# Optimization experiments

Measured on AMD Instinct MI355X. Metric: run time of the kernel, lower is better.

The kernel has to match this reference:

```python
import jax, jax.numpy as jnp
import numpy as np

MARKER = 50251
BETA_FLOOR = 0.1
LOCAL_SCALE = 0.3
EPS = 1e-6
WINDOW = 256

B, T, D, H, K, V = 4, 1024, 1024, 16, 64, 64
HD = D // H  # SWA head dim


def setup_inputs() -> dict:
    key = jax.random.key(0)
    ks = jax.random.split(key, 16)
    p = lambda i, shape: jax.random.normal(ks[i], shape, jnp.float32) * 0.02
    return dict(
        x=jax.random.normal(ks[0], (B, T, D), jnp.float32),
        initial_state=jnp.zeros((B, H, K, V), jnp.float32),
        W_k=p(1, (D, H * K)),
        W_v=p(2, (D, H * V)),
        W_gdn_o=p(3, (H * V, D)),
        W_beta=p(4, (D, H)), b_beta=jnp.full((H,), -2.0, jnp.float32),
        W_g=p(5, (D, H)), b_g=jnp.full((H,), 2.0, jnp.float32),
        W_lq=p(6, (D, D)), W_lk=p(7, (D, D)), W_lv=p(8, (D, D)),
        W_swa_o=p(9, (D, D)),
        W_ret_o=p(10, (H * V, D)),
        W_gate=p(11, (D, H)), b_gate=jnp.ones((H,), jnp.float32),
        norm_w=jnp.ones((D,), jnp.float32),
        input_ids=jax.random.randint(ks[12], (B, T), 0, 50257, jnp.int32),
    )


def _delta_scan(k, v, beta, g, S0):
    # gated delta rule:  Sd = g_t * S_{t-1};  S_t = Sd + beta_t * k_t (v_t - k_t Sd);  o_t = k_t S_t
    # k:[B,Tm,H,K]  v:[B,Tm,H,V]  beta,g:[B,Tm,H]  S0:[B,H,K,V]
    def step(S, inp):
        kt, vt, bt, gt = inp  # [B,H,K],[B,H,V],[B,H],[B,H]
        Sd = gt[..., None, None] * S
        err = vt - jnp.einsum('bhk,bhkv->bhv', kt, Sd)
        Sn = Sd + bt[..., None, None] * (kt[..., None] * err[:, :, None, :])
        ot = jnp.einsum('bhk,bhkv->bhv', kt, Sn)
        return Sn, ot
    Sf, o = jax.lax.scan(step, S0, (k.transpose(1, 0, 2, 3), v.transpose(1, 0, 2, 3),
                                    beta.transpose(1, 0, 2), g.transpose(1, 0, 2)))
    return o.transpose(1, 0, 2, 3), Sf  # [B,Tm,H,V], [B,H,K,V]


def _forward(x, initial_state, W_k, W_v, W_gdn_o, W_beta, b_beta, W_g, b_g,
             W_lq, W_lk, W_lv, W_swa_o, W_ret_o, W_gate, b_gate, norm_w, input_ids):
    # RMSNorm
    rms = jnp.sqrt(jnp.mean(x * x, axis=-1, keepdims=True) + EPS)
    xn = x / rms * norm_w

    # shared L2-normalized keys and values
    k_shared = (xn @ W_k).reshape(B, T, H, K)
    k_shared = k_shared / jnp.maximum(jnp.linalg.norm(k_shared, axis=-1, keepdims=True), 1e-12)
    v_full = (xn @ W_v).reshape(B, T, H, V)

    # shifted-value GDN inputs (predict next token's value)
    k = k_shared[:, :-1]
    v = v_full[:, 1:]
    beta = jax.nn.sigmoid(xn[:, :-1] @ W_beta + b_beta)  # [B,T-1,H]
    g = jax.nn.sigmoid(xn[:, :-1] @ W_g + b_g)
    marker = (input_ids[:, :-1] == MARKER)[..., None]
    beta = beta * (BETA_FLOOR + (1.0 - BETA_FLOOR) * marker.astype(beta.dtype))

    o, Sf = _delta_scan(k, v, beta, g, initial_state)
    gdn_out = jnp.concatenate([jnp.zeros((B, 1, H, V), o.dtype), o], axis=1)
    gdn_out = gdn_out.reshape(B, T, H * V) @ W_gdn_o  # [B,T,D]

    # sliding-window attention (fallback masked-softmax path)
    q = (xn @ W_lq).reshape(B, T, H, HD).transpose(0, 2, 1, 3)
    kl = (xn @ W_lk).reshape(B, T, H, HD).transpose(0, 2, 1, 3)
    vl = (xn @ W_lv).reshape(B, T, H, HD).transpose(0, 2, 1, 3)
    scale = K ** (-0.5)
    i = jnp.arange(T)[:, None]
    j = jnp.arange(T)[None, :]
    allowed = (j <= i) & (j >= i - WINDOW)  # causal within window
    attn = jnp.einsum('bhqd,bhkd->bhqk', q, kl) * scale
    attn = jnp.where(allowed, attn, -jnp.inf)
    probs = jax.nn.softmax(attn, axis=-1)
    local = jnp.einsum('bhqk,bhkd->bhqd', probs, vl).transpose(0, 2, 1, 3).reshape(B, T, D)
    local_out = LOCAL_SCALE * (local @ W_swa_o)  # eval mode

    # retrieval from final state with shared keys as queries
    retrieved = jnp.einsum('bhkv,bthk->bthv', Sf, k_shared).reshape(B, T, H * V)
    retrieval_out = retrieved @ W_ret_o
    gate = jax.nn.sigmoid(xn @ W_gate + b_gate)  # [B,T,H]
    retrieval_out = jnp.mean(gate, axis=-1, keepdims=True) * retrieval_out

    return x + gdn_out + local_out + retrieval_out


def reference(x, initial_state, W_k, W_v, W_gdn_o, W_beta, b_beta, W_g, b_g,
              W_lq, W_lk, W_lv, W_swa_o, W_ret_o, W_gate, b_gate, norm_w, input_ids):
    return _forward(x, initial_state, W_k, W_v, W_gdn_o, W_beta, b_beta, W_g, b_g,
                    W_lq, W_lk, W_lv, W_swa_o, W_ret_o, W_gate, b_gate, norm_w, input_ids)
```

## Files before the change

kernel.cpp:

```cpp
#include <hip/hip_runtime.h>
#include <hip/hip_bf16.h>

#define BB 4
#define TT 1024
#define DD 1024
#define HH 16
#define KK 64
#define VV 64
#define WIN 256
#define MARKER_ID 50251
#define PSA 5120
#define PSB 3072
#define NPROJ 5248

typedef short bfrag8 __attribute__((ext_vector_type(8)));
typedef float f32x4 __attribute__((ext_vector_type(4)));

static __device__ __forceinline__ unsigned short f2bf(float f) {
  __hip_bfloat16 h = __float2bfloat16(f);
  union { __hip_bfloat16 h; unsigned short u; } cv;
  cv.h = h;
  return cv.u;
}
static __device__ __forceinline__ float bf2f(unsigned short u) {
  union { unsigned int i; float f; } c;
  c.i = ((unsigned int)u) << 16;
  return c.f;
}
static __device__ __forceinline__ void gld_lds16(const unsigned short* g,
                                                 unsigned short* l) {
  __builtin_amdgcn_global_load_lds(
      (const __attribute__((address_space(1))) void*)g,
      (__attribute__((address_space(3))) void*)l, 16, 0, 0);
}

__global__ __launch_bounds__(256) void rmsnorm_kernel(
    const float* __restrict__ x, const float* __restrict__ nw,
    unsigned short* __restrict__ xnb) {
  int row = blockIdx.x;
  int tid = threadIdx.x;
  const float4* xr = (const float4*)(x + (size_t)row * DD);
  float4 v = xr[tid];
  float ss = v.x * v.x + v.y * v.y + v.z * v.z + v.w * v.w;
#pragma unroll
  for (int off = 32; off; off >>= 1) ss += __shfl_xor(ss, off);
  __shared__ float red[4];
  int wid = tid >> 6;
  if ((tid & 63) == 0) red[wid] = ss;
  __syncthreads();
  float tot = red[0] + red[1] + red[2] + red[3];
  float inv = 1.0f / sqrtf(tot * (1.0f / DD) + 1e-6f);
  const float4* wr = (const float4*)nw;
  float4 wv = wr[tid];
  ushort4 o;
  o.x = f2bf(v.x * inv * wv.x);
  o.y = f2bf(v.y * inv * wv.y);
  o.z = f2bf(v.z * inv * wv.z);
  o.w = f2bf(v.w * inv * wv.w);
  *(ushort4*)&xnb[(size_t)row * DD + tid * 4] = o;
}

__global__ __launch_bounds__(256) void convert_wt_kernel(
    const float* W0, const float* W1, const float* W2, const float* W3,
    const float* W4, const float* W5, const float* W6, const float* W7,
    const float* Wb, const float* Wg, const float* Wgt,
    unsigned short* C5, unsigned short* C3) {
  int tid = threadIdx.x;
  if (blockIdx.z == 8) {
    if (blockIdx.x != 0) return;
    int k0 = blockIdx.y * 64;
    for (int e = tid; e < 3 * 16 * 64; e += 256) {
      int w = e >> 10;
      int h = (e >> 6) & 15;
      int kk = e & 63;
      const float* Ws = (w == 0) ? Wb : (w == 1) ? Wg : Wgt;
      C5[(size_t)(5120 + w * 16 + h) * 1024 + k0 + kk] =
          f2bf(Ws[(size_t)(k0 + kk) * 16 + h]);
    }
    for (int e = tid; e < 80 * 64; e += 256) {
      int r = e >> 6, kk = e & 63;
      C5[(size_t)(5168 + r) * 1024 + k0 + kk] = 0;
    }
    return;
  }
  const float* W;
  unsigned short* T;
  int stride;
  float scale = 1.f;
  switch (blockIdx.z) {
    case 0: W = W0; T = C5 + 0 * 1024 * 1024; stride = 1024; break;
    case 1: W = W1; T = C5 + 1 * 1024 * 1024; stride = 1024; break;
    case 2: W = W2; T = C5 + 2 * 1024 * 1024; stride = 1024; break;
    case 3: W = W3; T = C5 + 3 * 1024 * 1024; stride = 1024; break;
    case 4: W = W4; T = C5 + 4 * 1024 * 1024; stride = 1024; break;
    case 5: W = W5; T = C3 + 0; stride = PSB; break;
    case 6: W = W6; T = C3 + 1024; stride = PSB; scale = 0.3f; break;
    default: W = W7; T = C3 + 2048; stride = PSB; break;
  }
  __shared__ float Ts[64][68];
  int n0 = blockIdx.x * 64, k0 = blockIdx.y * 64;
#pragma unroll
  for (int p = 0; p < 4; ++p) {
    int e = p * 256 + tid;
    int k = e >> 4, nq = e & 15;
    float4 w = *(const float4*)&W[(size_t)(k0 + k) * 1024 + n0 + nq * 4];
    Ts[nq * 4 + 0][k] = w.x;
    Ts[nq * 4 + 1][k] = w.y;
    Ts[nq * 4 + 2][k] = w.z;
    Ts[nq * 4 + 3][k] = w.w;
  }
  __syncthreads();
#pragma unroll
  for (int p = 0; p < 4; ++p) {
    int e = p * 256 + tid;
    int n = e >> 4, kq = e & 15;
    float4 v = *(const float4*)&Ts[n][kq * 4];
    ushort4 u;
    u.x = f2bf(v.x * scale);
    u.y = f2bf(v.y * scale);
    u.z = f2bf(v.z * scale);
    u.w = f2bf(v.w * scale);
    *(ushort4*)&T[(size_t)(n0 + n) * stride + k0 + kq * 4] = u;
  }
}

__global__ __launch_bounds__(256) void gemm_out_kernel(
    const unsigned short* __restrict__ A, const unsigned short* __restrict__ BT,
    float* __restrict__ C, const float* __restrict__ addp, int M, int N,
    int K) {
  __shared__ unsigned short As[2][128][32];
  __shared__ unsigned short Bs[2][64][32];
  int flat = blockIdx.y * gridDim.x + blockIdx.x;
  int xcd = flat & 7, local = flat >> 3;
  int m0 = (xcd * 4 + (local & 3)) * 128;
  int n0 = (local >> 2) * 64;
  int tid = threadIdx.x;
  int wave = tid >> 6, lane = tid & 63;
  int wm = wave * 32;
  int r16 = lane & 15, quad = lane >> 4;
  int lrow = lane >> 2, lcol = (lane & 3) * 8;

  f32x4 acc[2][4];
#pragma unroll
  for (int i = 0; i < 2; ++i)
#pragma unroll
    for (int j = 0; j < 4; ++j) acc[i][j] = {0.f, 0.f, 0.f, 0.f};

#pragma unroll
  for (int q = 0; q < 2; ++q) {
    int rb = (wave * 2 + q) * 16;
    gld_lds16(&A[(size_t)(m0 + rb + lrow) * K + lcol], &As[0][rb][0]);
  }
  {
    int rb = wave * 16;
    gld_lds16(&BT[(size_t)(n0 + rb + lrow) * K + lcol], &Bs[0][rb][0]);
  }
  __syncthreads();

  int cur = 0;
  for (int kt = 32; kt < K; kt += 32) {
#pragma unroll
    for (int q = 0; q < 2; ++q) {
      int rb = (wave * 2 + q) * 16;
      gld_lds16(&A[(size_t)(m0 + rb + lrow) * K + kt + lcol],
                &As[cur ^ 1][rb][0]);
    }
    {
      int rb = wave * 16;
      gld_lds16(&BT[(size_t)(n0 + rb + lrow) * K + kt + lcol],
                &Bs[cur ^ 1][rb][0]);
    }
    bfrag8 af[2], bq[4];
#pragma unroll
    for (int i = 0; i < 2; ++i)
      af[i] = *(const bfrag8*)&As[cur][wm + i * 16 + r16][quad * 8];
#pragma unroll
    for (int j = 0; j < 4; ++j)
      bq[j] = *(const bfrag8*)&Bs[cur][j * 16 + r16][quad * 8];
#pragma unroll
    for (int i = 0; i < 2; ++i)
#pragma unroll
      for (int j = 0; j < 4; ++j)
        acc[i][j] = __builtin_amdgcn_mfma_f32_16x16x32_bf16(af[i], bq[j],
                                                            acc[i][j], 0, 0, 0);
    __syncthreads();
    cur ^= 1;
  }
  {
    bfrag8 af[2], bq[4];
#pragma unroll
    for (int i = 0; i < 2; ++i)
      af[i] = *(const bfrag8*)&As[cur][wm + i * 16 + r16][quad * 8];
#pragma unroll
    for (int j = 0; j < 4; ++j)
      bq[j] = *(const bfrag8*)&Bs[cur][j * 16 + r16][quad * 8];
#pragma unroll
    for (int i = 0; i < 2; ++i)
#pragma unroll
      for (int j = 0; j < 4; ++j)
        acc[i][j] = __builtin_amdgcn_mfma_f32_16x16x32_bf16(af[i], bq[j],
                                                            acc[i][j], 0, 0, 0);
  }
#pragma unroll
  for (int i = 0; i < 2; ++i) {
#pragma unroll
    for (int r = 0; r < 4; ++r) {
      int row = m0 + wm + i * 16 + quad * 4 + r;
#pragma unroll
      for (int j = 0; j < 4; ++j) {
        int col = n0 + j * 16 + r16;
        size_t idx = (size_t)row * N + col;
        C[idx] = addp[idx] + acc[i][j][r];
      }
    }
  }
}

__global__ __launch_bounds__(256) void gemm_proj_kernel(
    const unsigned short* __restrict__ A, const unsigned short* __restrict__ BT,
    unsigned short* __restrict__ PALL, float* __restrict__ SPRJ) {
  const int K = 1024;
  __shared__ unsigned short As[2][128][32];
  __shared__ unsigned short Bs[2][128][32];
  int flat = blockIdx.y * gridDim.x + blockIdx.x;
  int xcd = flat & 7, local = flat >> 3;
  int mi = local & 3, ni = local >> 2;
  int m0 = (xcd * 4 + mi) * 128;
  int n0 = ni * 128;
  int tid = threadIdx.x;
  int wave = tid >> 6, lane = tid & 63;
  int wm = (wave & 1) * 64, wn = (wave >> 1) * 64;
  int r16 = lane & 15, quad = lane >> 4;
  int lrow = lane >> 2, lcol = (lane & 3) * 8;

  f32x4 acc[4][4];
#pragma unroll
  for (int i = 0; i < 4; ++i)
#pragma unroll
    for (int j = 0; j < 4; ++j) acc[i][j] = {0.f, 0.f, 0.f, 0.f};

#pragma unroll
  for (int q = 0; q < 2; ++q) {
    int rb = (wave * 2 + q) * 16;
    gld_lds16(&A[(size_t)(m0 + rb + lrow) * K + lcol], &As[0][rb][0]);
    gld_lds16(&BT[(size_t)(n0 + rb + lrow) * K + lcol], &Bs[0][rb][0]);
  }
  __syncthreads();

  int cur = 0;
  for (int kt = 32; kt < K; kt += 32) {
#pragma unroll
    for (int q = 0; q < 2; ++q) {
      int rb = (wave * 2 + q) * 16;
      gld_lds16(&A[(size_t)(m0 + rb + lrow) * K + kt + lcol],
                &As[cur ^ 1][rb][0]);
      gld_lds16(&BT[(size_t)(n0 + rb + lrow) * K + kt + lcol],
                &Bs[cur ^ 1][rb][0]);
    }
    bfrag8 af[4], bq[4];
#pragma unroll
    for (int i = 0; i < 4; ++i) {
      af[i] = *(const bfrag8*)&As[cur][wm + i * 16 + r16][quad * 8];
      bq[i] = *(const bfrag8*)&Bs[cur][wn + i * 16 + r16][quad * 8];
    }
#pragma unroll
    for (int i = 0; i < 4; ++i)
#pragma unroll
      for (int j = 0; j < 4; ++j)
        acc[i][j] = __builtin_amdgcn_mfma_f32_16x16x32_bf16(af[i], bq[j],
                                                            acc[i][j], 0, 0, 0);
    __syncthreads();
    cur ^= 1;
  }
  {
    bfrag8 af[4], bq[4];
#pragma unroll
    for (int i = 0; i < 4; ++i) {
      af[i] = *(const bfrag8*)&As[cur][wm + i * 16 + r16][quad * 8];
      bq[i] = *(const bfrag8*)&Bs[cur][wn + i * 16 + r16][quad * 8];
    }
#pragma unroll
    for (int i = 0; i < 4; ++i)
#pragma unroll
      for (int j = 0; j < 4; ++j)
        acc[i][j] = __builtin_amdgcn_mfma_f32_16x16x32_bf16(af[i], bq[j],
                                                            acc[i][j], 0, 0, 0);
  }
  bool gates = (n0 >= 5120);
#pragma unroll
  for (int i = 0; i < 4; ++i) {
#pragma unroll
    for (int r = 0; r < 4; ++r) {
      int row = m0 + wm + i * 16 + quad * 4 + r;
#pragma unroll
      for (int j = 0; j < 4; ++j) {
        int col = n0 + wn + j * 16 + r16;
        if (!gates)
          PALL[(size_t)row * PSA + col] = f2bf(acc[i][j][r]);
        else
          SPRJ[(size_t)row * 128 + col - 5120] = acc[i][j][r];
      }
    }
  }
}

__global__ __launch_bounds__(256) void gates_kernel(
    const float* __restrict__ SPRJ, const float* __restrict__ bb,
    const float* __restrict__ bg, const float* __restrict__ bgt,
    const int* __restrict__ ids, float* __restrict__ beta,
    float* __restrict__ g, float* __restrict__ mg) {
  int row = blockIdx.x * 4 + (threadIdx.x >> 6);
  int lane = threadIdx.x & 63;
  if (lane < 48) {
    int h = lane & 15;
    float v = SPRJ[(size_t)row * 128 + lane];
    float bias = (lane < 16) ? bb[h] : (lane < 32) ? bg[h] : bgt[h];
    float s = 1.f / (1.f + __expf(-(v + bias)));
    if (lane < 16) {
      float mk = (ids[row] == MARKER_ID) ? 1.f : 0.1f;
      beta[(size_t)row * 16 + h] = s * mk;
    } else if (lane < 32) {
      g[(size_t)row * 16 + h] = s;
    } else {
      float sum = s;
#pragma unroll
      for (int off = 1; off < 16; off <<= 1) sum += __shfl_xor(sum, off);
      if (lane == 32) mg[row] = sum * (1.f / 16.f);
    }
  }
}

__global__ __launch_bounds__(256) void knorm_kernel(
    unsigned short* __restrict__ pall) {
  int w = blockIdx.x * 4 + (threadIdx.x >> 6);
  int lane = threadIdx.x & 63;
  size_t addr = (size_t)(w >> 4) * PSA + (w & 15) * 64 + lane;
  float v = bf2f(pall[addr]);
  float ss = v * v;
#pragma unroll
  for (int off = 32; off; off >>= 1) ss += __shfl_xor(ss, off);
  float n = sqrtf(ss);
  n = fmaxf(n, 1e-12f);
  pall[addr] = f2bf(v / n);
}

__global__ __launch_bounds__(256) void attn_mfma_kernel(
    const unsigned short* __restrict__ PALL, unsigned short* __restrict__ ACAT) {
  __shared__ unsigned short Qs[64][72];
  __shared__ unsigned short Ks[64][72];
  __shared__ unsigned short Vt[64][72];
  __shared__ unsigned short Ps[64][72];
  int qb = blockIdx.x * 64;
  int bh = blockIdx.y;
  int h = bh & 15, b = bh >> 4;
  int tid = threadIdx.x, lane = tid & 63, wave = tid >> 6;
  int r16 = lane & 15, quad = lane >> 4;
  int m0w = wave * 16;
  const unsigned short* Qg = PALL + (size_t)b * TT * PSA + 2048 + h * 64;
  const unsigned short* Kg = Qg + 1024;
  const unsigned short* Vg = Qg + 2048;
  int sr = tid >> 2, sq = tid & 3;
  {
    *(uint4*)&Qs[sr][sq * 16] =
        *(const uint4*)&Qg[(size_t)(qb + sr) * PSA + sq * 16];
    *(uint4*)&Qs[sr][sq * 16 + 8] =
        *(const uint4*)&Qg[(size_t)(qb + sr) * PSA + sq * 16 + 8];
  }
  float m[4], l[4];
  f32x4 o[4];
#pragma unroll
  for (int r = 0; r < 4; ++r) {
    m[r] = -1e30f;
    l[r] = 0.f;
    o[r] = {0.f, 0.f, 0.f, 0.f};
  }
  int kt0 = qb - (int)WIN;
  if (kt0 < 0) kt0 = 0;

  for (int kt = kt0; kt <= qb; kt += 64) {
    __syncthreads();
    {
      *(uint4*)&Ks[sr][sq * 16] =
          *(const uint4*)&Kg[(size_t)(kt + sr) * PSA + sq * 16];
      *(uint4*)&Ks[sr][sq * 16 + 8] =
          *(const uint4*)&Kg[(size_t)(kt + sr) * PSA + sq * 16 + 8];
      union { uint4 u4[2]; unsigned short s[16]; } vv;
      vv.u4[0] = *(const uint4*)&Vg[(size_t)(kt + sr) * PSA + sq * 16];
      vv.u4[1] = *(const uint4*)&Vg[(size_t)(kt + sr) * PSA + sq * 16 + 8];
#pragma unroll
      for (int i = 0; i < 16; ++i) Vt[sq * 16 + i][sr] = vv.s[i];
    }
    __syncthreads();
    bfrag8 af0 = *(const bfrag8*)&Qs[m0w + r16][quad * 8];
    bfrag8 af1 = *(const bfrag8*)&Qs[m0w + r16][quad * 8 + 32];
    f32x4 s[4];
#pragma unroll
    for (int j = 0; j < 4; ++j) s[j] = {0.f, 0.f, 0.f, 0.f};
#pragma unroll
    for (int j = 0; j < 4; ++j) {
      bfrag8 b0 = *(const bfrag8*)&Ks[j * 16 + r16][quad * 8];
      bfrag8 b1 = *(const bfrag8*)&Ks[j * 16 + r16][quad * 8 + 32];
      s[j] = __builtin_amdgcn_mfma_f32_16x16x32_bf16(af0, b0, s[j], 0, 0, 0);
      s[j] = __builtin_amdgcn_mfma_f32_16x16x32_bf16(af1, b1, s[j], 0, 0, 0);
    }
    bool oldest = (kt == qb - (int)WIN);
    bool newest = (kt == qb);
#pragma unroll
    for (int r = 0; r < 4; ++r) {
      int il = m0w + quad * 4 + r;
      float sv[4];
#pragma unroll
      for (int j = 0; j < 4; ++j) {
        int jl = j * 16 + r16;
        float v = s[j][r] * 0.125f;
        if (oldest && jl < il) v = -1e30f;
        if (newest && jl > il) v = -1e30f;
        sv[j] = v;
      }
      float mx = fmaxf(fmaxf(sv[0], sv[1]), fmaxf(sv[2], sv[3]));
#pragma unroll
      for (int off = 1; off < 16; off <<= 1) mx = fmaxf(mx, __shfl_xor(mx, off));
      float mn = fmaxf(m[r], mx);
      float al = __expf(m[r] - mn);
      m[r] = mn;
      float rs = 0.f;
#pragma unroll
      for (int j = 0; j < 4; ++j) {
        float p = __expf(sv[j] - mn);
        rs += p;
        Ps[il][j * 16 + r16] = f2bf(p);
      }
#pragma unroll
      for (int off = 1; off < 16; off <<= 1) rs += __shfl_xor(rs, off);
      l[r] = l[r] * al + rs;
#pragma unroll
      for (int j = 0; j < 4; ++j) o[j][r] *= al;
    }
    bfrag8 pa0 = *(const bfrag8*)&Ps[m0w + r16][quad * 8];
    bfrag8 pa1 = *(const bfrag8*)&Ps[m0w + r16][quad * 8 + 32];
#pragma unroll
    for (int j = 0; j < 4; ++j) {
      bfrag8 v0 = *(const bfrag8*)&Vt[j * 16 + r16][quad * 8];
      bfrag8 v1 = *(const bfrag8*)&Vt[j * 16 + r16][quad * 8 + 32];
      o[j] = __builtin_amdgcn_mfma_f32_16x16x32_bf16(pa0, v0, o[j], 0, 0, 0);
      o[j] = __builtin_amdgcn_mfma_f32_16x16x32_bf16(pa1, v1, o[j], 0, 0, 0);
    }
  }
#pragma unroll
  for (int r = 0; r < 4; ++r) {
    int row = m0w + quad * 4 + r;
    float inv = 1.f / l[r];
#pragma unroll
    for (int j = 0; j < 4; ++j) {
      ACAT[((size_t)(b * TT + qb + row)) * PSB + 1024 + h * 64 + j * 16 + r16] =
          f2bf(o[j][r] * inv);
    }
  }
}

__global__ __launch_bounds__(256) void scan_phaseA(
    const unsigned short* __restrict__ PALL, const float* __restrict__ beta,
    const float* __restrict__ g, unsigned short* __restrict__ UFg,
    unsigned short* __restrict__ Zg, unsigned short* __restrict__ Pg,
    unsigned short* __restrict__ Qg, float* __restrict__ Ag) {
  __shared__ unsigned short Kc[64][72];
  __shared__ unsigned short KTb[64][72];
  __shared__ float Vc[64][68];
  __shared__ float Msv[64][68];
  __shared__ unsigned short UFT[64][72];
  __shared__ unsigned short ZTl[64][72];
  __shared__ float aArr[64], iaArr[64], bArr[64], baArr[64], sKT[64];
  __shared__ float aCs;

  int c = blockIdx.x, bh = blockIdx.y;
  int b = bh >> 4, h = bh & 15;
  int tc = c * 64;
  int tid = threadIdx.x, lane = tid & 63, wave = tid >> 6;
  int r16 = lane & 15, quad = lane >> 4;
  int m0w = wave * 16;
  size_t bhc = (size_t)bh * 16 + c;

  const unsigned short* kbase = PALL + ((size_t)b * TT) * PSA + h * 64;
  const unsigned short* vbase = kbase + 1024;
  const float* bbase = beta + ((size_t)b * TT) * HH + h;
  const float* gbase = g + ((size_t)b * TT) * HH + h;

  if (tid < 64) {
    int ts = tc + tid;
    bool pad = (ts > 1022);
    float gv = pad ? 1.f : gbase[(size_t)ts * HH];
    float bv = pad ? 0.f : bbase[(size_t)ts * HH];
    float p = gv;
#pragma unroll
    for (int o = 1; o < 64; o <<= 1) {
      float t = __shfl_up(p, o);
      if (lane >= o) p *= t;
    }
    aArr[tid] = p;
    iaArr[tid] = 1.f / p;
    bArr[tid] = bv;
    baArr[tid] = bv * p;
    float aC = __shfl(p, 63);
    sKT[tid] = aC / p;
    if (tid == 0) aCs = aC;
    Ag[bhc * 64 + tid] = p;
  }
  __syncthreads();
  {
    int r = tid >> 2, q = tid & 3;
    int ts = tc + r;
    float skt = sKT[r];
    union { uint4 u4[2]; unsigned short s[16]; } kv;
    kv.u4[0] = *(const uint4*)&kbase[(size_t)ts * PSA + q * 16];
    kv.u4[1] = *(const uint4*)&kbase[(size_t)ts * PSA + q * 16 + 8];
    *(uint4*)&Kc[r][q * 16] = kv.u4[0];
    *(uint4*)&Kc[r][q * 16 + 8] = kv.u4[1];
#pragma unroll
    for (int i = 0; i < 16; ++i)
      KTb[q * 16 + i][r] = f2bf(bf2f(kv.s[i]) * skt);
    if (ts <= 1022) {
      union { uint4 u4[2]; unsigned short s[16]; } vv;
      vv.u4[0] = *(const uint4*)&vbase[(size_t)(ts + 1) * PSA + q * 16];
      vv.u4[1] = *(const uint4*)&vbase[(size_t)(ts + 1) * PSA + q * 16 + 8];
#pragma unroll
      for (int i = 0; i < 16; ++i) Vc[r][q * 16 + i] = bf2f(vv.s[i]);
    } else {
#pragma unroll
      for (int i = 0; i < 16; ++i) Vc[r][q * 16 + i] = 0.f;
    }
  }
  __syncthreads();
  {
    bfrag8 af0 = *(const bfrag8*)&Kc[m0w + r16][quad * 8];
    bfrag8 af1 = *(const bfrag8*)&Kc[m0w + r16][quad * 8 + 32];
    f32x4 acc1[4];
#pragma unroll
    for (int j = 0; j < 4; ++j) acc1[j] = {0.f, 0.f, 0.f, 0.f};
#pragma unroll
    for (int j = 0; j < 4; ++j) {
      bfrag8 k0 = *(const bfrag8*)&Kc[j * 16 + r16][quad * 8];
      bfrag8 k1 = *(const bfrag8*)&Kc[j * 16 + r16][quad * 8 + 32];
      acc1[j] = __builtin_amdgcn_mfma_f32_16x16x32_bf16(af0, k0, acc1[j], 0, 0, 0);
      acc1[j] = __builtin_amdgcn_mfma_f32_16x16x32_bf16(af1, k1, acc1[j], 0, 0, 0);
    }
#pragma unroll
    for (int j = 0; j < 4; ++j) {
#pragma unroll
      for (int r = 0; r < 4; ++r) {
        int row = m0w + quad * 4 + r;
        int col = j * 16 + r16;
        Msv[row][col] =
            (col < row) ? bArr[row] * aArr[row] * iaArr[col] * acc1[j][r] : 0.f;
      }
    }
  }
  __syncthreads();
  if (wave < 2) {
    float u[64];
    if (wave == 0) {
#pragma unroll
      for (int t = 0; t < 64; ++t) u[t] = bArr[t] * Vc[t][lane];
    } else {
#pragma unroll
      for (int t = 0; t < 64; ++t) u[t] = baArr[t] * bf2f(Kc[t][lane]);
    }
#pragma unroll
    for (int t = 1; t < 64; ++t) {
      float a0 = 0.f, a1 = 0.f, a2 = 0.f, a3 = 0.f;
#pragma unroll
      for (int s4 = 0; s4 * 4 < t; ++s4) {
        float4 mr = *(const float4*)&Msv[t][s4 * 4];
        a0 = fmaf(mr.x, u[s4 * 4 + 0], a0);
        a1 = fmaf(mr.y, u[s4 * 4 + 1], a1);
        a2 = fmaf(mr.z, u[s4 * 4 + 2], a2);
        a3 = fmaf(mr.w, u[s4 * 4 + 3], a3);
      }
      u[t] -= (a0 + a1) + (a2 + a3);
    }
    unsigned short* Tls = (wave == 0) ? &UFT[lane][0] : &ZTl[lane][0];
#pragma unroll
    for (int t2 = 0; t2 < 32; ++t2) {
      unsigned int pk = (unsigned int)f2bf(u[2 * t2]) |
                        ((unsigned int)f2bf(u[2 * t2 + 1]) << 16);
      *(unsigned int*)&Tls[2 * t2] = pk;
    }
    unsigned short* Gn = (wave == 0) ? UFg : Zg;
#pragma unroll
    for (int t = 0; t < 64; ++t) {
      Gn[(bhc * 64 + t) * 64 + lane] = f2bf(u[t]);
    }
  }
  __syncthreads();
  {
    bfrag8 af0 = *(const bfrag8*)&KTb[m0w + r16][quad * 8];
    bfrag8 af1 = *(const bfrag8*)&KTb[m0w + r16][quad * 8 + 32];
    f32x4 accp[4], accq[4];
#pragma unroll
    for (int j = 0; j < 4; ++j) {
      accp[j] = {0.f, 0.f, 0.f, 0.f};
      accq[j] = {0.f, 0.f, 0.f, 0.f};
    }
#pragma unroll
    for (int j = 0; j < 4; ++j) {
      bfrag8 z0 = *(const bfrag8*)&ZTl[j * 16 + r16][quad * 8];
      bfrag8 z1 = *(const bfrag8*)&ZTl[j * 16 + r16][quad * 8 + 32];
      accp[j] = __builtin_amdgcn_mfma_f32_16x16x32_bf16(af0, z0, accp[j], 0, 0, 0);
      accp[j] = __builtin_amdgcn_mfma_f32_16x16x32_bf16(af1, z1, accp[j], 0, 0, 0);
      bfrag8 u0 = *(const bfrag8*)&UFT[j * 16 + r16][quad * 8];
      bfrag8 u1 = *(const bfrag8*)&UFT[j * 16 + r16][quad * 8 + 32];
      accq[j] = __builtin_amdgcn_mfma_f32_16x16x32_bf16(af0, u0, accq[j], 0, 0, 0);
      accq[j] = __builtin_amdgcn_mfma_f32_16x16x32_bf16(af1, u1, accq[j], 0, 0, 0);
    }
    float aC = aCs;
#pragma unroll
    for (int j = 0; j < 4; ++j) {
#pragma unroll
      for (int r = 0; r < 4; ++r) {
        int row = m0w + quad * 4 + r;
        int col = j * 16 + r16;
        float pv = ((row == col) ? aC : 0.f) - accp[j][r];
        Pg[bhc * 4096 + (size_t)row * 64 + col] = f2bf(pv);
        Qg[bhc * 4096 + (size_t)row * 64 + col] = f2bf(accq[j][r]);
      }
    }
  }
}

__global__ __launch_bounds__(256) void scan_phaseB(
    const float* __restrict__ S0, const unsigned short* __restrict__ Pg,
    const unsigned short* __restrict__ Qg, unsigned short* __restrict__ SinTg,
    float* __restrict__ Sf, unsigned short* __restrict__ ACAT) {
  __shared__ unsigned short STb[64][72];
  __shared__ unsigned short Pl[64][72];
  int bh = blockIdx.x;
  int b = bh >> 4, h = bh & 15;
  int tid = threadIdx.x, lane = tid & 63, wave = tid >> 6;
  int r16 = lane & 15, quad = lane >> 4;
  int m0w = wave * 16;
  int rr = tid >> 2, qq = tid & 3;
  {
    const float* s0p = S0 + (size_t)bh * 4096;
#pragma unroll
    for (int i = 0; i < 4; ++i) {
      float4 sv = *(const float4*)&s0p[rr * 64 + qq * 16 + i * 4];
      STb[qq * 16 + i * 4 + 0][rr] = f2bf(sv.x);
      STb[qq * 16 + i * 4 + 1][rr] = f2bf(sv.y);
      STb[qq * 16 + i * 4 + 2][rr] = f2bf(sv.z);
      STb[qq * 16 + i * 4 + 3][rr] = f2bf(sv.w);
    }
    if (tid < 64) ACAT[((size_t)b * TT) * PSB + h * 64 + tid] = 0;
  }
  for (int c = 0; c < 16; ++c) {
    size_t bhc = (size_t)bh * 16 + c;
    __syncthreads();
    {
      uint4 s0v = *(const uint4*)&STb[rr][qq * 16];
      uint4 s1v = *(const uint4*)&STb[rr][qq * 16 + 8];
      *(uint4*)&SinTg[bhc * 4096 + (size_t)rr * 64 + qq * 16] = s0v;
      *(uint4*)&SinTg[bhc * 4096 + (size_t)rr * 64 + qq * 16 + 8] = s1v;
      uint4 p0 = *(const uint4*)&Pg[bhc * 4096 + (size_t)rr * 64 + qq * 16];
      uint4 p1 = *(const uint4*)&Pg[bhc * 4096 + (size_t)rr * 64 + qq * 16 + 8];
      *(uint4*)&Pl[rr][qq * 16] = p0;
      *(uint4*)&Pl[rr][qq * 16 + 8] = p1;
    }
    __syncthreads();
    f32x4 acc[4];
#pragma unroll
    for (int j = 0; j < 4; ++j) acc[j] = {0.f, 0.f, 0.f, 0.f};
    {
      bfrag8 af0 = *(const bfrag8*)&Pl[m0w + r16][quad * 8];
      bfrag8 af1 = *(const bfrag8*)&Pl[m0w + r16][quad * 8 + 32];
#pragma unroll
      for (int j = 0; j < 4; ++j) {
        bfrag8 s0v = *(const bfrag8*)&STb[j * 16 + r16][quad * 8];
        bfrag8 s1v = *(const bfrag8*)&STb[j * 16 + r16][quad * 8 + 32];
        acc[j] = __builtin_amdgcn_mfma_f32_16x16x32_bf16(af0, s0v, acc[j], 0, 0, 0);
        acc[j] = __builtin_amdgcn_mfma_f32_16x16x32_bf16(af1, s1v, acc[j], 0, 0, 0);
      }
    }
    float snew[4][4];
#pragma unroll
    for (int j = 0; j < 4; ++j) {
#pragma unroll
      for (int r = 0; r < 4; ++r) {
        int row = m0w + quad * 4 + r;
        int col = j * 16 + r16;
        snew[j][r] = acc[j][r] + bf2f(Qg[bhc * 4096 + (size_t)row * 64 + col]);
      }
    }
    __syncthreads();
#pragma unroll
    for (int j = 0; j < 4; ++j) {
#pragma unroll
      for (int r = 0; r < 4; ++r) {
        int row = m0w + quad * 4 + r;
        int col = j * 16 + r16;
        STb[col][row] = f2bf(snew[j][r]);
        if (c == 15) Sf[(size_t)bh * 4096 + (size_t)row * 64 + col] = snew[j][r];
      }
    }
  }
}

__global__ __launch_bounds__(256) void scan_phaseC(
    const unsigned short* __restrict__ PALL,
    const unsigned short* __restrict__ UFg,
    const unsigned short* __restrict__ Zg,
    const unsigned short* __restrict__ SinTg, const float* __restrict__ Ag,
    unsigned short* __restrict__ ACAT) {
  __shared__ unsigned short Kc[64][72];
  __shared__ unsigned short SvT[64][72];
  __shared__ unsigned short Zl[64][72];
  __shared__ unsigned short Ufl[64][72];
  __shared__ unsigned short Wl[64][72];
  __shared__ unsigned short UTl[64][72];
  __shared__ float aA[64], iaA[64];

  int c = blockIdx.x, bh = blockIdx.y;
  int b = bh >> 4, h = bh & 15;
  int tc = c * 64;
  int tid = threadIdx.x, lane = tid & 63, wave = tid >> 6;
  int r16 = lane & 15, quad = lane >> 4;
  int m0w = wave * 16;
  size_t bhc = (size_t)bh * 16 + c;
  const unsigned short* kbase = PALL + ((size_t)b * TT) * PSA + h * 64;

  if (tid < 64) {
    float av = Ag[bhc * 64 + tid];
    aA[tid] = av;
    iaA[tid] = 1.f / av;
  }
  {
    int r = tid >> 2, q = tid & 3;
    int ts = tc + r;
    *(uint4*)&Kc[r][q * 16] = *(const uint4*)&kbase[(size_t)ts * PSA + q * 16];
    *(uint4*)&Kc[r][q * 16 + 8] =
        *(const uint4*)&kbase[(size_t)ts * PSA + q * 16 + 8];
    uint4 sv0 = *(const uint4*)&SinTg[bhc * 4096 + (size_t)r * 64 + q * 16];
    uint4 sv1 = *(const uint4*)&SinTg[bhc * 4096 + (size_t)r * 64 + q * 16 + 8];
    *(uint4*)&SvT[r][q * 16] = sv0;
    *(uint4*)&SvT[r][q * 16 + 8] = sv1;
    uint4 zv0 = *(const uint4*)&Zg[(bhc * 64 + r) * 64 + q * 16];
    uint4 zv1 = *(const uint4*)&Zg[(bhc * 64 + r) * 64 + q * 16 + 8];
    *(uint4*)&Zl[r][q * 16] = zv0;
    *(uint4*)&Zl[r][q * 16 + 8] = zv1;
    uint4 uv0 = *(const uint4*)&UFg[(bhc * 64 + r) * 64 + q * 16];
    uint4 uv1 = *(const uint4*)&UFg[(bhc * 64 + r) * 64 + q * 16 + 8];
    *(uint4*)&Ufl[r][q * 16] = uv0;
    *(uint4*)&Ufl[r][q * 16 + 8] = uv1;
  }
  __syncthreads();
  float op[4][4];
  {
    bfrag8 af0 = *(const bfrag8*)&Kc[m0w + r16][quad * 8];
    bfrag8 af1 = *(const bfrag8*)&Kc[m0w + r16][quad * 8 + 32];
    bfrag8 zf0 = *(const bfrag8*)&Zl[m0w + r16][quad * 8];
    bfrag8 zf1 = *(const bfrag8*)&Zl[m0w + r16][quad * 8 + 32];
    f32x4 acc1[4], acc2[4], acc3[4];
#pragma unroll
    for (int j = 0; j < 4; ++j) {
      acc1[j] = {0.f, 0.f, 0.f, 0.f};
      acc2[j] = {0.f, 0.f, 0.f, 0.f};
      acc3[j] = {0.f, 0.f, 0.f, 0.f};
    }
#pragma unroll
    for (int j = 0; j < 4; ++j) {
      bfrag8 k0 = *(const bfrag8*)&Kc[j * 16 + r16][quad * 8];
      bfrag8 k1 = *(const bfrag8*)&Kc[j * 16 + r16][quad * 8 + 32];
      acc1[j] = __builtin_amdgcn_mfma_f32_16x16x32_bf16(af0, k0, acc1[j], 0, 0, 0);
      acc1[j] = __builtin_amdgcn_mfma_f32_16x16x32_bf16(af1, k1, acc1[j], 0, 0, 0);
      bfrag8 s0 = *(const bfrag8*)&SvT[j * 16 + r16][quad * 8];
      bfrag8 s1 = *(const bfrag8*)&SvT[j * 16 + r16][quad * 8 + 32];
      acc3[j] = __builtin_amdgcn_mfma_f32_16x16x32_bf16(af0, s0, acc3[j], 0, 0, 0);
      acc3[j] = __builtin_amdgcn_mfma_f32_16x16x32_bf16(af1, s1, acc3[j], 0, 0, 0);
      acc2[j] = __builtin_amdgcn_mfma_f32_16x16x32_bf16(zf0, s0, acc2[j], 0, 0, 0);
      acc2[j] = __builtin_amdgcn_mfma_f32_16x16x32_bf16(zf1, s1, acc2[j], 0, 0, 0);
    }
#pragma unroll
    for (int j = 0; j < 4; ++j) {
#pragma unroll
      for (int r = 0; r < 4; ++r) {
        int row = m0w + quad * 4 + r;
        int col = j * 16 + r16;
        Wl[row][col] = (col <= row) ? f2bf(aA[row] * iaA[col] * acc1[j][r])
                                    : (unsigned short)0;
        float uval = bf2f(Ufl[row][col]) - acc2[j][r];
        UTl[col][row] = f2bf(uval);
        op[j][r] = aA[row] * acc3[j][r];
      }
    }
  }
  __syncthreads();
  {
    bfrag8 wf0 = *(const bfrag8*)&Wl[m0w + r16][quad * 8];
    bfrag8 wf1 = *(const bfrag8*)&Wl[m0w + r16][quad * 8 + 32];
    f32x4 acc4[4];
#pragma unroll
    for (int j = 0; j < 4; ++j) acc4[j] = {0.f, 0.f, 0.f, 0.f};
#pragma unroll
    for (int j = 0; j < 4; ++j) {
      bfrag8 u0 = *(const bfrag8*)&UTl[j * 16 + r16][quad * 8];
      bfrag8 u1 = *(const bfrag8*)&UTl[j * 16 + r16][quad * 8 + 32];
      acc4[j] = __builtin_amdgcn_mfma_f32_16x16x32_bf16(wf0, u0, acc4[j], 0, 0, 0);
      acc4[j] = __builtin_amdgcn_mfma_f32_16x16x32_bf16(wf1, u1, acc4[j], 0, 0, 0);
    }
#pragma unroll
    for (int j = 0; j < 4; ++j) {
#pragma unroll
      for (int r = 0; r < 4; ++r) {
        int row = m0w + quad * 4 + r;
        int col = j * 16 + r16;
        int ts = tc + row;
        if (ts < 1023) {
          ACAT[((size_t)b * TT + ts + 1) * PSB + h * 64 + col] =
              f2bf(op[j][r] + acc4[j][r]);
        }
      }
    }
  }
}

__global__ __launch_bounds__(256) void retrieve_kernel(
    const unsigned short* __restrict__ PALL, const float* __restrict__ Sf,
    const float* __restrict__ mg, unsigned short* __restrict__ ACAT) {
  int w = blockIdx.x * 4 + (threadIdx.x >> 6);
  int lane = threadIdx.x & 63;
  int bt = w >> 4;
  float kl = bf2f(PALL[(size_t)bt * PSA + (w & 15) * 64 + lane]);
  int b = bt >> 10;
  int bh = b * 16 + (w & 15);
  const float* sfp = Sf + (size_t)bh * 4096;
  float acc = 0.f;
#pragma unroll
  for (int k = 0; k < 64; ++k) {
    float kk = __shfl(kl, k);
    acc = fmaf(kk, sfp[k * 64 + lane], acc);
  }
  ACAT[(size_t)bt * PSB + 2048 + (w & 15) * 64 + lane] = f2bf(acc * mg[bt]);
}

extern "C" void kernel_launch(void* const* d_in, const int* in_sizes, int n_in,
                              void* d_out, int out_size, void* d_ws,
                              size_t ws_size, hipStream_t stream) {
  (void)in_sizes; (void)n_in; (void)out_size; (void)ws_size;
  const float* x       = (const float*)d_in[0];
  const float* S0      = (const float*)d_in[1];
  const float* W_k     = (const float*)d_in[2];
  const float* W_v     = (const float*)d_in[3];
  const float* W_gdn_o = (const float*)d_in[4];
  const float* W_beta  = (const float*)d_in[5];
  const float* b_beta  = (const float*)d_in[6];
  const float* W_g     = (const float*)d_in[7];
  const float* b_g     = (const float*)d_in[8];
  const float* W_lq    = (const float*)d_in[9];
  const float* W_lk    = (const float*)d_in[10];
  const float* W_lv    = (const float*)d_in[11];
  const float* W_swa_o = (const float*)d_in[12];
  const float* W_ret_o = (const float*)d_in[13];
  const float* W_gate  = (const float*)d_in[14];
  const float* b_gate  = (const float*)d_in[15];
  const float* norm_w  = (const float*)d_in[16];
  const int*   ids     = (const int*)d_in[17];
  float* out = (float*)d_out;

  char* ws = (char*)d_ws;
  size_t off = 0;
  auto allocf = [&](size_t n) {
    float* p = (float*)(ws + off);
    off += n * sizeof(float);
    return p;
  };
  auto allocu = [&](size_t n) {
    unsigned short* p = (unsigned short*)(ws + off);
    off += n * sizeof(unsigned short);
    return p;
  };
  const int M = BB * TT;
  unsigned short* XNb    = allocu((size_t)M * DD);
  unsigned short* PALL   = allocu((size_t)M * PSA);
  unsigned short* ACAT   = allocu((size_t)M * PSB);
  float*          SPRJ   = allocf((size_t)M * 128);
  unsigned short* WTcat5 = allocu((size_t)NPROJ * 1024);
  unsigned short* WTcat3 = allocu((size_t)1024 * PSB);
  float* BETA = allocf((size_t)M * HH);
  float* Gg   = allocf((size_t)M * HH);
  float* MG   = allocf((size_t)M);
  float* SF   = allocf((size_t)BB * HH * KK * VV);
  const size_t CH = (size_t)BB * HH * 16 * 64 * 64;
  unsigned short* UFg   = allocu(CH);
  unsigned short* Zg    = allocu(CH);
  unsigned short* Pg    = allocu(CH);
  unsigned short* Qg    = allocu(CH);
  unsigned short* SinTg = allocu(CH);
  float* Ag = allocf((size_t)BB * HH * 16 * 64);

  rmsnorm_kernel<<<M, 256, 0, stream>>>(x, norm_w, XNb);

  convert_wt_kernel<<<dim3(16, 16, 9), 256, 0, stream>>>(
      W_k, W_v, W_lq, W_lk, W_lv, W_gdn_o, W_swa_o, W_ret_o, W_beta, W_g,
      W_gate, WTcat5, WTcat3);

  gemm_proj_kernel<<<dim3(41, 32), 256, 0, stream>>>(XNb, WTcat5, PALL, SPRJ);

  knorm_kernel<<<(M * HH) / 4, 256, 0, stream>>>(PALL);
  gates_kernel<<<M / 4, 256, 0, stream>>>(SPRJ, b_beta, b_g, b_gate, ids, BETA,
                                          Gg, MG);

  scan_phaseA<<<dim3(16, BB * HH), 256, 0, stream>>>(PALL, BETA, Gg, UFg, Zg,
                                                     Pg, Qg, Ag);
  scan_phaseB<<<BB * HH, 256, 0, stream>>>(S0, Pg, Qg, SinTg, SF, ACAT);
  scan_phaseC<<<dim3(16, BB * HH), 256, 0, stream>>>(PALL, UFg, Zg, SinTg, Ag,
                                                     ACAT);

  attn_mfma_kernel<<<dim3(TT / 64, BB * HH), 256, 0, stream>>>(PALL, ACAT);

  retrieve_kernel<<<(M * HH) / 4, 256, 0, stream>>>(PALL, SF, MG, ACAT);

  gemm_out_kernel<<<dim3(16, 32), 256, 0, stream>>>(ACAT, WTcat3, out, x, M, DD,
                                                    3072);
}
```

Baseline: 403.7 us.

## Fuse key L2-norm and gate sigmoids into projection GEMM epilogue; pipeline output GEMM

The projection GEMM epilogue now L2-normalizes the shared-key columns in registers and computes the beta, g and mean-gate sigmoids directly from the accumulators. This removes the separate knorm and gates kernels and the SPRJ round trip. Normalizing from fp32 accumulators before rounding to bf16 slightly changes numerics versus normalizing after rounding. The output GEMM loop is also restructured to prefetch two stages ahead, using explicit vmcnt waits and raw barriers to overlap global loads with MFMA.

```diff
diff --git a/kernel.cpp b/kernel.cpp
--- a/kernel.cpp
+++ b/kernel.cpp
@@ -146,61 +146,55 @@
 #pragma unroll
     for (int j = 0; j < 4; ++j) acc[i][j] = {0.f, 0.f, 0.f, 0.f};
 
-#pragma unroll
-  for (int q = 0; q < 2; ++q) {
-    int rb = (wave * 2 + q) * 16;
-    gld_lds16(&A[(size_t)(m0 + rb + lrow) * K + lcol], &As[0][rb][0]);
-  }
-  {
-    int rb = wave * 16;
-    gld_lds16(&BT[(size_t)(n0 + rb + lrow) * K + lcol], &Bs[0][rb][0]);
-  }
-  __syncthreads();
-
-  int cur = 0;
-  for (int kt = 32; kt < K; kt += 32) {
+  auto STAGE = [&](int buf, int kt) {
 #pragma unroll
     for (int q = 0; q < 2; ++q) {
       int rb = (wave * 2 + q) * 16;
-      gld_lds16(&A[(size_t)(m0 + rb + lrow) * K + kt + lcol],
-                &As[cur ^ 1][rb][0]);
+      gld_lds16(&A[(size_t)(m0 + rb + lrow) * K + kt + lcol], &As[buf][rb][0]);
     }
     {
       int rb = wave * 16;
-      gld_lds16(&BT[(size_t)(n0 + rb + lrow) * K + kt + lcol],
-                &Bs[cur ^ 1][rb][0]);
-    }
+      gld_lds16(&BT[(size_t)(n0 + rb + lrow) * K + kt + lcol], &Bs[buf][rb][0]);
+    }
+  };
+  auto COMPUTE = [&](int buf) {
     bfrag8 af[2], bq[4];
 #pragma unroll
     for (int i = 0; i < 2; ++i)
-      af[i] = *(const bfrag8*)&As[cur][wm + i * 16 + r16][quad * 8];
+      af[i] = *(const bfrag8*)&As[buf][wm + i * 16 + r16][quad * 8];
 #pragma unroll
     for (int j = 0; j < 4; ++j)
-      bq[j] = *(const bfrag8*)&Bs[cur][j * 16 + r16][quad * 8];
+      bq[j] = *(const bfrag8*)&Bs[buf][j * 16 + r16][quad * 8];
 #pragma unroll
     for (int i = 0; i < 2; ++i)
 #pragma unroll
       for (int j = 0; j < 4; ++j)
         acc[i][j] = __builtin_amdgcn_mfma_f32_16x16x32_bf16(af[i], bq[j],
                                                             acc[i][j], 0, 0, 0);
-    __syncthreads();
+  };
+
+  STAGE(0, 0);
+  STAGE(1, 32);
+  asm volatile("s_waitcnt vmcnt(3)" ::: "memory");
+  __builtin_amdgcn_s_barrier();
+  __builtin_amdgcn_sched_barrier(0);
+
+  int cur = 0;
+  for (int kt = 64; kt < K; kt += 32) {
+    COMPUTE(cur);
+    __builtin_amdgcn_s_barrier();
+    STAGE(cur, kt);
+    asm volatile("s_waitcnt vmcnt(3)" ::: "memory");
+    __builtin_amdgcn_s_barrier();
+    __builtin_amdgcn_sched_barrier(0);
     cur ^= 1;
   }
-  {
-    bfrag8 af[2], bq[4];
-#pragma unroll
-    for (int i = 0; i < 2; ++i)
-      af[i] = *(const bfrag8*)&As[cur][wm + i * 16 + r16][quad * 8];
-#pragma unroll
-    for (int j = 0; j < 4; ++j)
-      bq[j] = *(const bfrag8*)&Bs[cur][j * 16 + r16][quad * 8];
-#pragma unroll
-    for (int i = 0; i < 2; ++i)
-#pragma unroll
-      for (int j = 0; j < 4; ++j)
-        acc[i][j] = __builtin_amdgcn_mfma_f32_16x16x32_bf16(af[i], bq[j],
-                                                            acc[i][j], 0, 0, 0);
-  }
+  COMPUTE(cur);
+  asm volatile("s_waitcnt vmcnt(0)" ::: "memory");
+  __builtin_amdgcn_s_barrier();
+  __builtin_amdgcn_sched_barrier(0);
+  COMPUTE(cur ^ 1);
+
 #pragma unroll
   for (int i = 0; i < 2; ++i) {
 #pragma unroll
@@ -218,7 +212,10 @@
 
 __global__ __launch_bounds__(256) void gemm_proj_kernel(
     const unsigned short* __restrict__ A, const unsigned short* __restrict__ BT,
-    unsigned short* __restrict__ PALL, float* __restrict__ SPRJ) {
+    unsigned short* __restrict__ PALL, const float* __restrict__ bb,
+    const float* __restrict__ bg, const float* __restrict__ bgt,
+    const int* __restrict__ ids, float* __restrict__ BETA,
+    float* __restrict__ Gg, float* __restrict__ MG) {
   const int K = 1024;
   __shared__ unsigned short As[2][128][32];
   __shared__ unsigned short Bs[2][128][32];
@@ -286,62 +283,57 @@
         acc[i][j] = __builtin_amdgcn_mfma_f32_16x16x32_bf16(af[i], bq[j],
                                                             acc[i][j], 0, 0, 0);
   }
+
   bool gates = (n0 >= 5120);
-#pragma unroll
-  for (int i = 0; i < 4; ++i) {
-#pragma unroll
-    for (int r = 0; r < 4; ++r) {
-      int row = m0 + wm + i * 16 + quad * 4 + r;
-#pragma unroll
-      for (int j = 0; j < 4; ++j) {
-        int col = n0 + wn + j * 16 + r16;
-        if (!gates)
+  if (!gates) {
+    bool donorm = (n0 < 1024);
+    if (donorm) {
+#pragma unroll
+      for (int i = 0; i < 4; ++i) {
+#pragma unroll
+        for (int r = 0; r < 4; ++r) {
+          float ss = 0.f;
+#pragma unroll
+          for (int j = 0; j < 4; ++j) ss += acc[i][j][r] * acc[i][j][r];
+#pragma unroll
+          for (int off = 1; off < 16; off <<= 1) ss += __shfl_xor(ss, off);
+          float inv = 1.0f / fmaxf(sqrtf(ss), 1e-12f);
+#pragma unroll
+          for (int j = 0; j < 4; ++j) acc[i][j][r] *= inv;
+        }
+      }
+    }
+#pragma unroll
+    for (int i = 0; i < 4; ++i) {
+#pragma unroll
+      for (int r = 0; r < 4; ++r) {
+        int row = m0 + wm + i * 16 + quad * 4 + r;
+#pragma unroll
+        for (int j = 0; j < 4; ++j) {
+          int col = n0 + wn + j * 16 + r16;
           PALL[(size_t)row * PSA + col] = f2bf(acc[i][j][r]);
-        else
-          SPRJ[(size_t)row * 128 + col - 5120] = acc[i][j][r];
-      }
-    }
-  }
-}
-
-__global__ __launch_bounds__(256) void gates_kernel(
-    const float* __restrict__ SPRJ, const float* __restrict__ bb,
-    const float* __restrict__ bg, const float* __restrict__ bgt,
-    const int* __restrict__ ids, float* __restrict__ beta,
-    float* __restrict__ g, float* __restrict__ mg) {
-  int row = blockIdx.x * 4 + (threadIdx.x >> 6);
-  int lane = threadIdx.x & 63;
-  if (lane < 48) {
-    int h = lane & 15;
-    float v = SPRJ[(size_t)row * 128 + lane];
-    float bias = (lane < 16) ? bb[h] : (lane < 32) ? bg[h] : bgt[h];
-    float s = 1.f / (1.f + __expf(-(v + bias)));
-    if (lane < 16) {
-      float mk = (ids[row] == MARKER_ID) ? 1.f : 0.1f;
-      beta[(size_t)row * 16 + h] = s * mk;
-    } else if (lane < 32) {
-      g[(size_t)row * 16 + h] = s;
-    } else {
-      float sum = s;
-#pragma unroll
-      for (int off = 1; off < 16; off <<= 1) sum += __shfl_xor(sum, off);
-      if (lane == 32) mg[row] = sum * (1.f / 16.f);
-    }
-  }
-}
-
-__global__ __launch_bounds__(256) void knorm_kernel(
-    unsigned short* __restrict__ pall) {
-  int w = blockIdx.x * 4 + (threadIdx.x >> 6);
-  int lane = threadIdx.x & 63;
-  size_t addr = (size_t)(w >> 4) * PSA + (w & 15) * 64 + lane;
-  float v = bf2f(pall[addr]);
-  float ss = v * v;
-#pragma unroll
-  for (int off = 32; off; off >>= 1) ss += __shfl_xor(ss, off);
-  float n = sqrtf(ss);
-  n = fmaxf(n, 1e-12f);
-  pall[addr] = f2bf(v / n);
+        }
+      }
+    }
+  } else if (wn == 0) {
+#pragma unroll
+    for (int i = 0; i < 4; ++i) {
+#pragma unroll
+      for (int r = 0; r < 4; ++r) {
+        int row = m0 + wm + i * 16 + quad * 4 + r;
+        float mk = (ids[row] == MARKER_ID) ? 1.f : 0.1f;
+        float sb = 1.f / (1.f + __expf(-(acc[i][0][r] + bb[r16])));
+        BETA[(size_t)row * 16 + r16] = sb * mk;
+        float sg = 1.f / (1.f + __expf(-(acc[i][1][r] + bg[r16])));
+        Gg[(size_t)row * 16 + r16] = sg;
+        float st = 1.f / (1.f + __expf(-(acc[i][2][r] + bgt[r16])));
+        float sum = st;
+#pragma unroll
+        for (int off = 1; off < 16; off <<= 1) sum += __shfl_xor(sum, off);
+        if (r16 == 0) MG[row] = sum * (1.f / 16.f);
+      }
+    }
+  }
 }
 
 __global__ __launch_bounds__(256) void attn_mfma_kernel(
@@ -879,7 +871,6 @@
   unsigned short* XNb    = allocu((size_t)M * DD);
   unsigned short* PALL   = allocu((size_t)M * PSA);
   unsigned short* ACAT   = allocu((size_t)M * PSB);
-  float*          SPRJ   = allocf((size_t)M * 128);
   unsigned short* WTcat5 = allocu((size_t)NPROJ * 1024);
   unsigned short* WTcat3 = allocu((size_t)1024 * PSB);
   float* BETA = allocf((size_t)M * HH);
@@ -900,11 +891,8 @@
       W_k, W_v, W_lq, W_lk, W_lv, W_gdn_o, W_swa_o, W_ret_o, W_beta, W_g,
       W_gate, WTcat5, WTcat3);
 
-  gemm_proj_kernel<<<dim3(41, 32), 256, 0, stream>>>(XNb, WTcat5, PALL, SPRJ);
-
-  knorm_kernel<<<(M * HH) / 4, 256, 0, stream>>>(PALL);
-  gates_kernel<<<M / 4, 256, 0, stream>>>(SPRJ, b_beta, b_g, b_gate, ids, BETA,
-                                          Gg, MG);
+  gemm_proj_kernel<<<dim3(41, 32), 256, 0, stream>>>(
+      XNb, WTcat5, PALL, b_beta, b_g, b_gate, ids, BETA, Gg, MG);
 
   scan_phaseA<<<dim3(16, BB * HH), 256, 0, stream>>>(PALL, BETA, Gg, UFg, Zg,
                                                      Pg, Qg, Ag);
```

Result: no change. 402.0 us (-0.4%).
